# Kernel tuning notes

Hardware: AMD Instinct MI355X
Metric: run time of the kernel (lower is better)

Reference implementation:

```python
import jax, jax.numpy as jnp
import numpy as np

B, N, D_IN, D_HID = 8, 2048, 512, 512

def setup_inputs() -> dict:
    key = jax.random.key(0)
    k1, k2, k3 = jax.random.split(key, 3)
    inp = jax.random.normal(k1, (B, N, D_IN), dtype=jnp.float32)
    # nn.Linear(input_size, hidden_size): weight [hidden, in], bias [hidden]
    W = jax.random.normal(k2, (D_HID, D_IN), dtype=jnp.float32) * (1.0 / np.sqrt(D_IN))
    b = jax.random.normal(k3, (D_HID,), dtype=jnp.float32) * 0.01
    return {"input": inp, "W": W, "b": b}

def reference(input, W, b):
    # x = fc(input): [B, N, D_HID]
    x = jnp.einsum('bnd,hd->bnh', input, W) + b
    # scores = x @ x^T (NO scale factor, matching the original): [B, N, N]
    scores = jnp.einsum('bnh,bmh->bnm', x, x)
    attn = jax.nn.softmax(scores, axis=2)
    # output = attn @ raw input (V = input, not the projection): [B, N, D_IN]
    output = jnp.einsum('bnm,bmd->bnd', attn, input)
    return output
```

## Files before the change

kernel.cpp:

```cpp
#include <hip/hip_runtime.h>
#include <hip/hip_bf16.h>
#include <stdint.h>

typedef short vbf16x8 __attribute__((ext_vector_type(8)));
typedef float vf32x4 __attribute__((ext_vector_type(4)));
typedef unsigned short u16;

__device__ __forceinline__ float bf2f(u16 u) {
  union { unsigned int i; float f; } v; v.i = ((unsigned int)u) << 16; return v.f;
}
__device__ __forceinline__ u16 f2bf(float f) {
  union { float f; unsigned int i; } v; v.f = f;
  return (u16)((v.i + 0x7fffu + ((v.i >> 16) & 1u)) >> 16);
}
__device__ __forceinline__ void gld16(const void* g, void* l) {
  __builtin_amdgcn_global_load_lds((const __attribute__((address_space(1))) void*)g,
                                   (__attribute__((address_space(3))) void*)l, 16, 0, 0);
}
template<int N> __device__ __forceinline__ void wait_vmcnt() {
  asm volatile("s_waitcnt vmcnt(%0)" :: "n"(N) : "memory");
}
__device__ __forceinline__ vbf16x8 ldsv(const u16* p) { return *(const vbf16x8*)p; }

__global__ __launch_bounds__(256) void k_convw(const float* __restrict__ W, u16* __restrict__ Wb) {
  int i = blockIdx.x * 256 + threadIdx.x;
  float4 x = ((const float4*)W)[i];
  ushort4 h;
  h.x = f2bf(x.x); h.y = f2bf(x.y); h.z = f2bf(x.z); h.w = f2bf(x.w);
  ((ushort4*)Wb)[i] = h;
}

__global__ __launch_bounds__(256) void k_prep(const float* __restrict__ in,
                                              u16* __restrict__ Abf, u16* __restrict__ Vt) {
  __shared__ u16 Ts[64][72];
  const int tid = threadIdx.x;
  const int n0 = blockIdx.x * 64, d0 = blockIdx.y * 64, b = blockIdx.z;
  const float* src = in + ((long long)b * 2048 + n0) * 512 + d0;
#pragma unroll
  for (int j = 0; j < 4; ++j) {
    int chunk = tid + 256 * j;
    int r = chunk >> 4, c = (chunk & 15) * 4;
    float4 x = *(const float4*)(src + (long long)r * 512 + c);
    ushort4 h;
    h.x = f2bf(x.x); h.y = f2bf(x.y); h.z = f2bf(x.z); h.w = f2bf(x.w);
    *(ushort4*)(Abf + ((long long)b * 2048 + n0 + r) * 512 + d0 + c) = h;
    Ts[c + 0][r] = h.x; Ts[c + 1][r] = h.y; Ts[c + 2][r] = h.z; Ts[c + 3][r] = h.w;
  }
  __syncthreads();
#pragma unroll
  for (int j = 0; j < 2; ++j) {
    int chunk = tid + 256 * j;
    int dr = chunk >> 3, c8 = (chunk & 7) * 8;
    vbf16x8 w = *(const vbf16x8*)&Ts[dr][c8];
    *(vbf16x8*)(Vt + ((long long)b * 512 + d0 + dr) * 2048 + n0 + c8) = w;
  }
}

__device__ __forceinline__ void sround(const u16* g, int K, int k0, u16* ldsbuf,
                                       int r, int srow, int scol, int wv) {
  gld16(g + (long long)(r * 64 + srow) * K + k0 + scol, ldsbuf + r * 4096 + wv * 512);
}

template<bool OUTBF, bool BIAS, int MAP>
__global__ __launch_bounds__(512, 2) void k_gemm(const u16* __restrict__ A,
                                                 const u16* __restrict__ Bt,
                                                 const float* __restrict__ bias,
                                                 void* __restrict__ Cout,
                                                 int M, int N, int K,
                                                 long long sA, long long sB, long long sC) {
  __shared__ __align__(16) u16 As[3 * 16384];
  __shared__ __align__(16) u16 Bs[3 * 8192];

  const int tid = threadIdx.x, lane = tid & 63, wv = tid >> 6;
  const int wr = wv >> 2, wc = wv & 3;

  const int lin = blockIdx.x;
  const int xcd = lin & 7, idx = lin >> 3;
  int zb, browi, bcoli;
  if constexpr (MAP == 1) { zb = 0; browi = xcd * 8 + (idx >> 2); bcoli = idx & 3; }
  else { zb = xcd; browi = idx >> 2; bcoli = idx & 3; }
  const int brow = browi * 256, bcol = bcoli * 128;
  const long long z = zb;

  const u16* gA = A + z * sA + (long long)brow * K;
  const u16* gB = Bt + z * sB + (long long)bcol * K;
  const int NT = K >> 6;

  const int srow = wv * 8 + (lane >> 3);
  const int scol = (((lane & 7) ^ ((lane >> 3) & 7)) << 3);
  const int rd0 = (lane & 15) * 64 + ((((lane >> 4)) ^ (lane & 7)) << 3);
  const int wrb = wr * 8192;
  const int wcb = wc * 2048;

  vf32x4 acc[8][2] = {};
  vbf16x8 afr[4], bfr[2];

  u16 *A0 = As, *A1 = As + 16384, *A2 = As + 32768;
  u16 *B0 = Bs, *B1 = Bs + 8192, *B2 = Bs + 16384;

  sround(gA, K, 0, A0, 0, srow, scol, wv);
  sround(gA, K, 0, A0, 1, srow, scol, wv);
  sround(gA, K, 0, A0, 2, srow, scol, wv);
  sround(gA, K, 0, A0, 3, srow, scol, wv);
  sround(gB, K, 0, B0, 0, srow, scol, wv);
  sround(gB, K, 0, B0, 1, srow, scol, wv);
  sround(gA, K, 64, A1, 0, srow, scol, wv);
  sround(gA, K, 64, A1, 1, srow, scol, wv);
  sround(gA, K, 64, A1, 2, srow, scol, wv);
  sround(gA, K, 64, A1, 3, srow, scol, wv);
  sround(gB, K, 64, B1, 0, srow, scol, wv);
  sround(gB, K, 64, B1, 1, srow, scol, wv);

  for (int t = 0; t < NT; ++t) {
    const int k2 = (t + 2) * 64;
    const bool st = (t + 2 < NT);

    if (t < NT - 1) wait_vmcnt<6>(); else wait_vmcnt<0>();
    __builtin_amdgcn_sched_barrier(0);
    __builtin_amdgcn_s_barrier();
    __builtin_amdgcn_sched_barrier(0);

#pragma unroll
    for (int n = 0; n < 2; ++n) bfr[n] = ldsv(B0 + wcb + n * 1024 + rd0);
#pragma unroll
    for (int i = 0; i < 4; ++i) afr[i] = ldsv(A0 + wrb + i * 1024 + rd0);
    if (st) { sround(gA, K, k2, A2, 0, srow, scol, wv); sround(gA, K, k2, A2, 1, srow, scol, wv); }
    __builtin_amdgcn_s_setprio(1);
#pragma unroll
    for (int i = 0; i < 4; ++i)
#pragma unroll
      for (int n = 0; n < 2; ++n)
        acc[i][n] = __builtin_amdgcn_mfma_f32_16x16x32_bf16(afr[i], bfr[n], acc[i][n], 0, 0, 0);
    __builtin_amdgcn_s_setprio(0);

#pragma unroll
    for (int i = 0; i < 4; ++i) afr[i] = ldsv(A0 + wrb + (4 + i) * 1024 + rd0);
    if (st) sround(gA, K, k2, A2, 2, srow, scol, wv);
    __builtin_amdgcn_s_setprio(1);
#pragma unroll
    for (int i = 0; i < 4; ++i)
#pragma unroll
      for (int n = 0; n < 2; ++n)
        acc[4 + i][n] = __builtin_amdgcn_mfma_f32_16x16x32_bf16(afr[i], bfr[n], acc[4 + i][n], 0, 0, 0);
    __builtin_amdgcn_s_setprio(0);

#pragma unroll
    for (int n = 0; n < 2; ++n) bfr[n] = ldsv(B0 + wcb + n * 1024 + (rd0 ^ 32));
#pragma unroll
    for (int i = 0; i < 4; ++i) afr[i] = ldsv(A0 + wrb + i * 1024 + (rd0 ^ 32));
    if (st) { sround(gA, K, k2, A2, 3, srow, scol, wv); sround(gB, K, k2, B2, 0, srow, scol, wv); }
    __builtin_amdgcn_s_setprio(1);
#pragma unroll
    for (int i = 0; i < 4; ++i)
#pragma unroll
      for (int n = 0; n < 2; ++n)
        acc[i][n] = __builtin_amdgcn_mfma_f32_16x16x32_bf16(afr[i], bfr[n], acc[i][n], 0, 0, 0);
    __builtin_amdgcn_s_setprio(0);

#pragma unroll
    for (int i = 0; i < 4; ++i) afr[i] = ldsv(A0 + wrb + (4 + i) * 1024 + (rd0 ^ 32));
    if (st) sround(gB, K, k2, B2, 1, srow, scol, wv);
    __builtin_amdgcn_s_setprio(1);
#pragma unroll
    for (int i = 0; i < 4; ++i)
#pragma unroll
      for (int n = 0; n < 2; ++n)
        acc[4 + i][n] = __builtin_amdgcn_mfma_f32_16x16x32_bf16(afr[i], bfr[n], acc[4 + i][n], 0, 0, 0);
    __builtin_amdgcn_s_setprio(0);

    u16* ta = A0; A0 = A1; A1 = A2; A2 = ta;
    u16* tb = B0; B0 = B1; B1 = B2; B2 = tb;
  }

  const long long zc = z * sC;
#pragma unroll
  for (int m = 0; m < 8; ++m) {
    const int row0 = brow + wr * 128 + m * 16 + (lane >> 4) * 4;
#pragma unroll
    for (int n = 0; n < 2; ++n) {
      const int col = bcol + wc * 32 + n * 16 + (lane & 15);
      const float bv = BIAS ? bias[col] : 0.0f;
#pragma unroll
      for (int r = 0; r < 4; ++r) {
        const float v = acc[m][n][r] + bv;
        const long long off = zc + (long long)(row0 + r) * N + col;
        if (OUTBF) ((u16*)Cout)[off] = f2bf(v);
        else       ((float*)Cout)[off] = v;
      }
    }
  }
}

__device__ __forceinline__ void sr32(const u16* g, int K, int k0, u16* ldsbuf,
                                     int r, int srow, int scol, int wv) {
  gld16(g + (long long)(r * 128 + srow) * K + k0 + scol, ldsbuf + r * 4096 + wv * 512);
}

__global__ __launch_bounds__(512, 2) void k_gemmS(const u16* __restrict__ X,
                                                  u16* __restrict__ P) {
  constexpr int K = 512, N = 2048;
  __shared__ __align__(16) u16 As[3 * 8192];
  __shared__ __align__(16) u16 Bs[3 * 8192];

  const int tid = threadIdx.x, lane = tid & 63, wv = tid >> 6;
  const int wr = wv >> 2, wc = wv & 3;

  const int lin = blockIdx.x;
  const int xcd = lin & 7, idx = lin >> 3;
  const int brow = (idx >> 3) * 256, bcol = (idx & 7) * 256;
  const long long z = xcd;

  const u16* gA = X + z * (2048LL * 512) + (long long)brow * K;
  const u16* gB = X + z * (2048LL * 512) + (long long)bcol * K;
  const int NT = K >> 5;

  const int srow = wv * 16 + (lane >> 2);
  const int scol = (((lane & 3) ^ ((lane >> 2) & 3)) << 3);

  const int rd = (lane & 15) * 32 + ((((lane >> 4)) ^ (lane & 3)) << 3);
  const int wrb = wr * 4096;
  const int wcb = wc * 2048;

  vf32x4 acc[8][4] = {};
  vbf16x8 afr[4], bfr[4];

  u16 *A0 = As, *A1 = As + 8192, *A2 = As + 16384;
  u16 *B0 = Bs, *B1 = Bs + 8192, *B2 = Bs + 16384;

  sr32(gA, K, 0, A0, 0, srow, scol, wv);
  sr32(gA, K, 0, A0, 1, srow, scol, wv);
  sr32(gB, K, 0, B0, 0, srow, scol, wv);
  sr32(gB, K, 0, B0, 1, srow, scol, wv);
  sr32(gA, K, 32, A1, 0, srow, scol, wv);
  sr32(gA, K, 32, A1, 1, srow, scol, wv);
  sr32(gB, K, 32, B1, 0, srow, scol, wv);
  sr32(gB, K, 32, B1, 1, srow, scol, wv);

  for (int t = 0; t < NT; ++t) {
    const int k2 = (t + 2) * 32;
    const bool st = (t + 2 < NT);

    if (t < NT - 1) wait_vmcnt<4>(); else wait_vmcnt<0>();
    __builtin_amdgcn_sched_barrier(0);
    __builtin_amdgcn_s_barrier();
    __builtin_amdgcn_sched_barrier(0);

#pragma unroll
    for (int n = 0; n < 4; ++n) bfr[n] = ldsv(B0 + wcb + n * 512 + rd);
#pragma unroll
    for (int i = 0; i < 4; ++i) afr[i] = ldsv(A0 + wrb + i * 512 + rd);
    if (st) { sr32(gA, K, k2, A2, 0, srow, scol, wv); sr32(gA, K, k2, A2, 1, srow, scol, wv); }
    __builtin_amdgcn_s_setprio(1);
#pragma unroll
    for (int i = 0; i < 4; ++i)
#pragma unroll
      for (int n = 0; n < 4; ++n)
        acc[i][n] = __builtin_amdgcn_mfma_f32_16x16x32_bf16(afr[i], bfr[n], acc[i][n], 0, 0, 0);
    __builtin_amdgcn_s_setprio(0);

#pragma unroll
    for (int i = 0; i < 4; ++i) afr[i] = ldsv(A0 + wrb + (4 + i) * 512 + rd);
    if (st) { sr32(gB, K, k2, B2, 0, srow, scol, wv); sr32(gB, K, k2, B2, 1, srow, scol, wv); }
    __builtin_amdgcn_s_setprio(1);
#pragma unroll
    for (int i = 0; i < 4; ++i)
#pragma unroll
      for (int n = 0; n < 4; ++n)
        acc[4 + i][n] = __builtin_amdgcn_mfma_f32_16x16x32_bf16(afr[i], bfr[n], acc[4 + i][n], 0, 0, 0);
    __builtin_amdgcn_s_setprio(0);

    u16* ta = A0; A0 = A1; A1 = A2; A2 = ta;
    u16* tb = B0; B0 = B1; B1 = B2; B2 = tb;
  }

  const long long zc = z * (2048LL * 2048);
#pragma unroll
  for (int m = 0; m < 8; ++m) {
    const int row0 = brow + wr * 128 + m * 16 + (lane >> 4) * 4;
#pragma unroll
    for (int n = 0; n < 4; ++n) {
      const int col = bcol + wc * 64 + n * 16 + (lane & 15);
#pragma unroll
      for (int r = 0; r < 4; ++r) {
        P[zc + (long long)(row0 + r) * N + col] = f2bf(acc[m][n][r]);
      }
    }
  }
}

__global__ __launch_bounds__(256) void k_softmax(u16* __restrict__ P) {
  const long long row = blockIdx.x;
  u16* p = P + row * 2048;
  const int tid = threadIdx.x, lane = tid & 63, wv = tid >> 6;
  vbf16x8 v = ((const vbf16x8*)p)[tid];
  float f[8];
#pragma unroll
  for (int j = 0; j < 8; ++j) f[j] = bf2f((u16)v[j]);
  float m = f[0];
#pragma unroll
  for (int j = 1; j < 8; ++j) m = fmaxf(m, f[j]);
  for (int o = 1; o < 64; o <<= 1) m = fmaxf(m, __shfl_xor(m, o));
  __shared__ float redm[4], reds[4];
  if (lane == 0) redm[wv] = m;
  __syncthreads();
  m = fmaxf(fmaxf(redm[0], redm[1]), fmaxf(redm[2], redm[3]));
  float s = 0.0f;
#pragma unroll
  for (int j = 0; j < 8; ++j) { f[j] = __expf(f[j] - m); s += f[j]; }
  for (int o = 1; o < 64; o <<= 1) s += __shfl_xor(s, o);
  if (lane == 0) reds[wv] = s;
  __syncthreads();
  const float inv = 1.0f / (reds[0] + reds[1] + reds[2] + reds[3]);
#pragma unroll
  for (int j = 0; j < 8; ++j) v[j] = (short)f2bf(f[j] * inv);
  ((vbf16x8*)p)[tid] = v;
}

extern "C" void kernel_launch(void* const* d_in, const int* in_sizes, int n_in,
                              void* d_out, int out_size, void* d_ws, size_t ws_size,
                              hipStream_t stream) {
  const float* input = (const float*)d_in[0];
  const float* W     = (const float*)d_in[1];
  const float* bias  = (const float*)d_in[2];
  float* out = (float*)d_out;

  char* ws = (char*)d_ws;
  u16* Xbf = (u16*)(ws);
  u16* Vt  = (u16*)(ws + 16777216);
  u16* P   = (u16*)(ws + 2LL * 16777216);
  u16* Abf = (u16*)(ws + 2LL * 16777216);
  u16* Wb  = (u16*)(ws + 3LL * 16777216);

  k_convw<<<256, 256, 0, stream>>>(W, Wb);
  k_prep<<<dim3(32, 8, 8), 256, 0, stream>>>(input, Abf, Vt);
  k_gemm<true, true, 1><<<256, 512, 0, stream>>>(
      Abf, Wb, bias, Xbf, 16384, 512, 512, 0, 0, 0);
  k_gemmS<<<512, 512, 0, stream>>>(Xbf, P);
  k_softmax<<<16384, 256, 0, stream>>>(P);
  k_gemm<false, false, 2><<<256, 512, 0, stream>>>(
      P, Vt, nullptr, out, 2048, 512, 2048,
      2048LL * 2048, 512LL * 2048, 2048LL * 512);
}
```

Before: 123.4 us.

## Switch S-GEMM from triple to double LDS buffering and change swizzle pattern

The score GEMM kernel drops from three LDS stages to two, prefetching one K-step ahead and waiting for all outstanding loads each iteration. All four tile loads for the next step are issued right after the barrier. The XOR swizzle used for LDS stores and fragment reads also changes to a different bank-mapping pattern. This halves LDS use, which can help occupancy, but it shortens the prefetch distance and may expose more global-load latency.

```diff
diff --git a/kernel.cpp b/kernel.cpp
--- a/kernel.cpp
+++ b/kernel.cpp
@@ -199,8 +199,8 @@
 __global__ __launch_bounds__(512, 2) void k_gemmS(const u16* __restrict__ X,
                                                   u16* __restrict__ P) {
   constexpr int K = 512, N = 2048;
-  __shared__ __align__(16) u16 As[3 * 8192];
-  __shared__ __align__(16) u16 Bs[3 * 8192];
+  __shared__ __align__(16) u16 As[2 * 8192];
+  __shared__ __align__(16) u16 Bs[2 * 8192];
 
   const int tid = threadIdx.x, lane = tid & 63, wv = tid >> 6;
   const int wr = wv >> 2, wc = wv & 3;
@@ -215,41 +215,45 @@
   const int NT = K >> 5;
 
   const int srow = wv * 16 + (lane >> 2);
-  const int scol = (((lane & 3) ^ ((lane >> 2) & 3)) << 3);
-
-  const int rd = (lane & 15) * 32 + ((((lane >> 4)) ^ (lane & 3)) << 3);
+  const int scol = (((lane & 3) ^ ((lane >> 3) & 3)) << 3);
+
+  const int rd = (lane & 15) * 32 + ((((lane >> 4)) ^ (((lane & 15) >> 1) & 3)) << 3);
   const int wrb = wr * 4096;
   const int wcb = wc * 2048;
 
   vf32x4 acc[8][4] = {};
   vbf16x8 afr[4], bfr[4];
 
-  u16 *A0 = As, *A1 = As + 8192, *A2 = As + 16384;
-  u16 *B0 = Bs, *B1 = Bs + 8192, *B2 = Bs + 16384;
-
-  sr32(gA, K, 0, A0, 0, srow, scol, wv);
-  sr32(gA, K, 0, A0, 1, srow, scol, wv);
-  sr32(gB, K, 0, B0, 0, srow, scol, wv);
-  sr32(gB, K, 0, B0, 1, srow, scol, wv);
-  sr32(gA, K, 32, A1, 0, srow, scol, wv);
-  sr32(gA, K, 32, A1, 1, srow, scol, wv);
-  sr32(gB, K, 32, B1, 0, srow, scol, wv);
-  sr32(gB, K, 32, B1, 1, srow, scol, wv);
+  sr32(gA, K, 0, As, 0, srow, scol, wv);
+  sr32(gA, K, 0, As, 1, srow, scol, wv);
+  sr32(gB, K, 0, Bs, 0, srow, scol, wv);
+  sr32(gB, K, 0, Bs, 1, srow, scol, wv);
 
   for (int t = 0; t < NT; ++t) {
-    const int k2 = (t + 2) * 32;
-    const bool st = (t + 2 < NT);
-
-    if (t < NT - 1) wait_vmcnt<4>(); else wait_vmcnt<0>();
+    const int buf = t & 1;
+    const u16* Ar = As + buf * 8192;
+    const u16* Br = Bs + buf * 8192;
+    u16* Ad = As + (buf ^ 1) * 8192;
+    u16* Bd = Bs + (buf ^ 1) * 8192;
+    const int k1 = (t + 1) * 32;
+    const bool st = (t + 1 < NT);
+
+    wait_vmcnt<0>();
     __builtin_amdgcn_sched_barrier(0);
     __builtin_amdgcn_s_barrier();
     __builtin_amdgcn_sched_barrier(0);
 
-#pragma unroll
-    for (int n = 0; n < 4; ++n) bfr[n] = ldsv(B0 + wcb + n * 512 + rd);
-#pragma unroll
-    for (int i = 0; i < 4; ++i) afr[i] = ldsv(A0 + wrb + i * 512 + rd);
-    if (st) { sr32(gA, K, k2, A2, 0, srow, scol, wv); sr32(gA, K, k2, A2, 1, srow, scol, wv); }
+    if (st) {
+      sr32(gA, K, k1, Ad, 0, srow, scol, wv);
+      sr32(gA, K, k1, Ad, 1, srow, scol, wv);
+      sr32(gB, K, k1, Bd, 0, srow, scol, wv);
+      sr32(gB, K, k1, Bd, 1, srow, scol, wv);
+    }
+
+#pragma unroll
+    for (int n = 0; n < 4; ++n) bfr[n] = ldsv(Br + wcb + n * 512 + rd);
+#pragma unroll
+    for (int i = 0; i < 4; ++i) afr[i] = ldsv(Ar + wrb + i * 512 + rd);
     __builtin_amdgcn_s_setprio(1);
 #pragma unroll
     for (int i = 0; i < 4; ++i)
@@ -259,8 +263,7 @@
     __builtin_amdgcn_s_setprio(0);
 
 #pragma unroll
-    for (int i = 0; i < 4; ++i) afr[i] = ldsv(A0 + wrb + (4 + i) * 512 + rd);
-    if (st) { sr32(gB, K, k2, B2, 0, srow, scol, wv); sr32(gB, K, k2, B2, 1, srow, scol, wv); }
+    for (int i = 0; i < 4; ++i) afr[i] = ldsv(Ar + wrb + (4 + i) * 512 + rd);
     __builtin_amdgcn_s_setprio(1);
 #pragma unroll
     for (int i = 0; i < 4; ++i)
@@ -268,9 +271,6 @@
       for (int n = 0; n < 4; ++n)
         acc[4 + i][n] = __builtin_amdgcn_mfma_f32_16x16x32_bf16(afr[i], bfr[n], acc[4 + i][n], 0, 0, 0);
     __builtin_amdgcn_s_setprio(0);
-
-    u16* ta = A0; A0 = A1; A1 = A2; A2 = ta;
-    u16* tb = B0; B0 = B1; B1 = B2; B2 = tb;
   }
 
   const long long zc = z * (2048LL * 2048);
```

Result: slower. 131.1 us (+6.3%).
